# Kernel tuning notes

Measured on AMD Instinct MI355X. Metric: run time of the kernel, lower is better.

The kernel has to match this reference:

```python
import jax, jax.numpy as jnp
import numpy as np

B, D, H, W, L = 32, 768, 14, 14, 77
TEMP_G, TEMP1, TEMP2, TEMP3 = 10.0, 4.0, 5.0, 10.0
LAMBDA_G, LAMBDA_L = 1.0, 1.0
EPS = 1e-8
NEG = -1e30


def setup_inputs() -> dict:
    key = jax.random.key(0)
    k1, k2, k3, k4, k5 = jax.random.split(key, 5)
    img_global = jax.random.normal(k1, (B, D), dtype=jnp.float32)
    img_local = jax.random.normal(k2, (B, D, H, W), dtype=jnp.float32)
    text_global = jax.random.normal(k3, (B, D), dtype=jnp.float32)
    text_local = jax.random.normal(k4, (B, L, D), dtype=jnp.float32)
    # ragged caption lengths: prefix attention mask, lengths in [10, L]
    lens = jax.random.randint(k5, (B,), 10, L + 1)
    attention_mask = (jnp.arange(L)[None, :] < lens[:, None]).astype(jnp.int32)
    return {"img_global": img_global, "img_local": img_local,
            "text_global": text_global, "text_local": text_local,
            "attention_mask": attention_mask}


def _ce_arange(scores):
    # cross entropy with labels = arange(n), mean reduction
    return jnp.mean(jax.nn.logsumexp(scores, axis=1) - jnp.diagonal(scores))


def _gloria_loss(img_global, img_local, text_global, text_local, attention_mask):
    mask = attention_mask.astype(bool)                      # [B, L]
    # ---- global contrastive loss ----
    in_ = img_global / jnp.maximum(jnp.linalg.norm(img_global, axis=1, keepdims=True), 1e-12)
    tn_ = text_global / jnp.maximum(jnp.linalg.norm(text_global, axis=1, keepdims=True), 1e-12)
    g_scores = (in_ @ tn_.T) * TEMP_G                       # [B, B]
    loss_global = 0.5 * (_ce_arange(g_scores) + _ce_arange(g_scores.T))

    # ---- local contrastive loss (vectorized over all text/image pairs) ----
    tl = jnp.swapaxes(text_local, 1, 2)                     # [B, D, L] (forward() transposes since L != D)
    ctx = img_local.reshape(B, D, H * W)                    # [B, D, S]
    # raw attention logits: text i words vs image j pixels -> [i, j, s, l]
    logits = jnp.einsum('jds,idl->ijsl', ctx, tl)
    logits = jnp.where(mask[:, None, None, :], logits, NEG)
    a1 = jax.nn.softmax(logits, axis=-1)                    # softmax over words (first softmax)
    a2 = jax.nn.softmax(TEMP1 * jnp.swapaxes(a1, 2, 3), axis=-1)  # [i, j, l, s], softmax over pixels
    wctx = jnp.einsum('jds,ijls->ijdl', ctx, a2)            # weighted context [i, j, D, l]
    # cosine similarity per word, over feature dim
    w12 = jnp.einsum('idl,ijdl->ijl', tl, wctx)
    n1 = jnp.linalg.norm(tl, axis=1)                        # [i, l]
    n2 = jnp.linalg.norm(wctx, axis=2)                      # [i, j, l]
    cos = w12 / jnp.maximum(n1[:, None, :] * n2, EPS)       # [i, j, l]
    row = jnp.exp(TEMP2 * cos) * mask[:, None, :]           # mask padded words
    sim = jnp.log(row.sum(axis=-1))                         # [i, j]  (local_agg='sum')
    # torch cats per-caption columns: similarities[j, i] -> transpose
    scores = sim.T * TEMP3                                  # [img j, text i]
    loss_local = 0.5 * (_ce_arange(scores) + _ce_arange(scores.T))

    return LAMBDA_G * loss_global + LAMBDA_L * loss_local


def reference(img_global, img_local, text_global, text_local, attention_mask):
    return _gloria_loss(img_global, img_local, text_global, text_local, attention_mask)
```

## Files before the change

kernel.cpp:

```cpp
#include <hip/hip_runtime.h>
#include <math.h>

#define NB 32
#define ND 768
#define NS 196
#define NL 77

typedef __bf16 bf16x8 __attribute__((ext_vector_type(8)));
typedef float f32x4 __attribute__((ext_vector_type(4)));

__device__ __forceinline__ f32x4 mfma16(bf16x8 a, bf16x8 b, f32x4 c) {
  return __builtin_amdgcn_mfma_f32_16x16x32_bf16(a, b, c, 0, 0, 0);
}

#define GLOAD16(gp, lp)                                          \
  __builtin_amdgcn_global_load_lds(                              \
      (const __attribute__((address_space(1))) void*)(gp),       \
      (__attribute__((address_space(3))) void*)(lp), 16, 0, 0)


__global__ __launch_bounds__(256) void prep_all_kernel(
    const float* __restrict__ text_local,
    const float* __restrict__ img_local,
    const int* __restrict__ amask,
    __bf16* __restrict__ txf, __bf16* __restrict__ cTf,
    float* __restrict__ n1ws, int* __restrict__ lenws) {
  const int bid = blockIdx.x;
  const int t = threadIdx.x;
  __shared__ float tile[32][213];

  if (bid < 960) {
    int tau = bid * 256 + t;
    int i = tau / 7680;
    int r = tau - i * 7680;
    int dk = r / 320;
    int r2 = r - dk * 320;
    int lt = r2 >> 6, lane = r2 & 63;
    int n16 = lane & 15, g = lane >> 4;
    int l = lt * 16 + n16;
    float v[8];
#pragma unroll
    for (int q = 0; q < 8; ++q) v[q] = 0.f;
    if (l < NL) {
      const float* src = text_local + ((size_t)i * NL + l) * ND + dk * 32 + g * 8;
      float4 a = *(const float4*)src;
      float4 b = *(const float4*)(src + 4);
      v[0] = a.x; v[1] = a.y; v[2] = a.z; v[3] = a.w;
      v[4] = b.x; v[5] = b.y; v[6] = b.z; v[7] = b.w;
    }
    bf16x8 hv, lv;
#pragma unroll
    for (int q = 0; q < 8; ++q) {
      __bf16 h = (__bf16)v[q];
      hv[q] = h;
      lv[q] = (__bf16)(v[q] - (float)h);
    }
    size_t base = ((((size_t)i * 24 + dk) * 5 + lt) * 2) * 512 + (size_t)lane * 8;
    *(bf16x8*)(txf + base) = hv;
    *(bf16x8*)(txf + base + 512) = lv;
  } else if (bid < 1344) {
    const int b2 = bid - 960;
    const int j = b2 / 12, dc = b2 - (b2 / 12) * 12;
    const float* src = img_local + ((size_t)j * ND + dc * 64) * NS;
#pragma unroll 1
    for (int h = 0; h < 2; ++h) {
      __syncthreads();
      for (int idx = t; idx < 1568; idx += 256) {
        int dd = idx / 49, sq = idx - dd * 49;
        float4 v = *(const float4*)(src + (size_t)(h * 32 + dd) * NS + sq * 4);
        tile[dd][sq * 4 + 0] = v.x;
        tile[dd][sq * 4 + 1] = v.y;
        tile[dd][sq * 4 + 2] = v.z;
        tile[dd][sq * 4 + 3] = v.w;
      }
      __syncthreads();
      const int dk = dc * 2 + h;
      for (int idx = t; idx < 832; idx += 256) {
        int lane = idx & 63;
        int S = idx >> 6;
        int n16 = lane & 15, g = lane >> 4;
        int s = S * 16 + n16;
        bf16x8 hv, lv;
#pragma unroll
        for (int e = 0; e < 8; ++e) {
          float v = (s < NS) ? tile[g * 8 + e][s] : 0.f;
          __bf16 hh = (__bf16)v;
          hv[e] = hh;
          lv[e] = (__bf16)(v - (float)hh);
        }
        size_t base = ((((size_t)j * 13 + S) * 24 + dk) * 2) * 512 + (size_t)lane * 8;
        *(bf16x8*)(cTf + base) = hv;
        *(bf16x8*)(cTf + base + 512) = lv;
      }
    }
  } else {
    const int i = bid - 1344;
    const int lane = t & 63, w = t >> 6;
    __shared__ int slen;
    if (t == 0) slen = 0;
    __syncthreads();
    if (t < NL && amask[i * NL + t] != 0) atomicAdd(&slen, 1);
    for (int l = w; l < NL; l += 4) {
      const float4* p = (const float4*)(text_local + ((size_t)i * NL + l) * ND);
      float s = 0.f;
#pragma unroll
      for (int k = 0; k < 3; ++k) {
        float4 v = p[lane + 64 * k];
        s += v.x * v.x + v.y * v.y + v.z * v.z + v.w * v.w;
      }
#pragma unroll
      for (int off = 32; off; off >>= 1) s += __shfl_xor(s, off);
      if (lane == 0) n1ws[i * 80 + l] = sqrtf(s);
    }
    __syncthreads();
    if (t == 0) lenws[i] = slen;
  }
}

__global__ void mid_kernel(const __bf16* __restrict__ cTf, __bf16* __restrict__ Gf,
                           const float* __restrict__ img_global,
                           const float* __restrict__ text_global,
                           float* __restrict__ gscw,
                           const int* __restrict__ lenws, int* __restrict__ ordws) {
  const int bid = blockIdx.x;
  const int t = threadIdx.x;
  __shared__ __align__(16) float shi[ND];

  if (bid < 832) {
    const int j = bid / 26;
    const int rr = bid - j * 26;
    const int st = rr >> 1, ch = rr & 1;
    const int lane = t & 63, w = t >> 6;
    const int g = lane >> 4, n16 = lane & 15;
    const f32x4 z4 = {0.f, 0.f, 0.f, 0.f};
    f32x4 accG[2];
    accG[0] = z4; accG[1] = z4;
    const int base = ch * 7;
    const int ncols = ch ? 6 : 7;
    const size_t cj = (size_t)j * 13;
    for (int dk = 0; dk < 24; ++dk) {
      size_t ao = ((cj + st) * 24 + dk) * 2 * 512 + (size_t)lane * 8;
      bf16x8 Ah = *(const bf16x8*)(cTf + ao);
      bf16x8 Al = *(const bf16x8*)(cTf + ao + 512);
#pragma unroll
      for (int q = 0; q < 2; ++q) {
        int ntl = w + (q << 2);
        if (ntl < ncols) {
          int nt = base + ntl;
          size_t bo = ((cj + nt) * 24 + dk) * 2 * 512 + (size_t)lane * 8;
          bf16x8 Bh = *(const bf16x8*)(cTf + bo);
          bf16x8 Bl = *(const bf16x8*)(cTf + bo + 512);
          accG[q] = mfma16(Ah, Bh, accG[q]);
          accG[q] = mfma16(Ah, Bl, accG[q]);
          accG[q] = mfma16(Al, Bh, accG[q]);
        }
      }
    }
#pragma unroll
    for (int q = 0; q < 2; ++q) {
      int ntl = w + (q << 2);
      int nt = base + ntl;
      bool compute = (ntl < ncols);
      bool zfill = (ch == 1 && nt == 13);
      if (compute || zfill) {
#pragma unroll
        for (int r = 0; r < 4; ++r) {
          int col = nt * 16 + n16;
          float v = compute ? accG[q][r] : 0.f;
          __bf16 hi = (__bf16)v;
          __bf16 lo = (__bf16)(v - (float)hi);
          int kt = col >> 5, gg = (col >> 3) & 3, e = col & 7;
          int lane2 = (g * 4 + r) + (gg << 4);
          size_t o = ((((size_t)j * 13 + st) * 7 + kt) * 2) * 512 + (size_t)lane2 * 8 + e;
          Gf[o] = hi;
          Gf[o + 512] = lo;
        }
      }
    }
  } else if (bid < 864) {
    const int a = bid - 832;
    const int lane = t & 63, w = t >> 6;
    if (t < ND / 4) ((float4*)shi)[t] = ((const float4*)(img_global + (size_t)a * ND))[t];
    __syncthreads();
    for (int b = w; b < NB; b += 4) {
      const float4* pt = (const float4*)(text_global + (size_t)b * ND);
      const float4* pi = (const float4*)shi;
      float dot = 0.f, ni = 0.f, nt = 0.f;
#pragma unroll
      for (int k = 0; k < 3; ++k) {
        float4 x = pi[lane + 64 * k];
        float4 y = pt[lane + 64 * k];
        dot += x.x * y.x + x.y * y.y + x.z * y.z + x.w * y.w;
        ni  += x.x * x.x + x.y * x.y + x.z * x.z + x.w * x.w;
        nt  += y.x * y.x + y.y * y.y + y.z * y.z + y.w * y.w;
      }
#pragma unroll
      for (int off = 32; off; off >>= 1) {
        dot += __shfl_xor(dot, off);
        ni  += __shfl_xor(ni, off);
        nt  += __shfl_xor(nt, off);
      }
      if (lane == 0)
        gscw[a * NB + b] = dot / fmaxf(sqrtf(ni), 1e-12f) / fmaxf(sqrtf(nt), 1e-12f) * 10.0f;
    }
  } else {
    if (t == 0) {
      int o[32];
      for (int k = 0; k < 32; ++k) o[k] = k;
      for (int x = 0; x < 31; ++x) {
        int best = x;
        for (int y = x + 1; y < 32; ++y)
          if (lenws[o[y]] > lenws[o[best]]) best = y;
        int tmp = o[x]; o[x] = o[best]; o[best] = tmp;
      }
      for (int k = 0; k < 32; ++k) ordws[k] = o[k];
    }
  }
}

__global__ __launch_bounds__(512, 3) void pair_kernel(
    const __bf16* __restrict__ txf, const __bf16* __restrict__ cTf,
    const __bf16* __restrict__ Gf,
    const float* __restrict__ n1ws, const int* __restrict__ lenws,
    const int* __restrict__ ordws,
    float* __restrict__ simws) {
  const int t = threadIdx.x;
  const int wg = ((blockIdx.x & 7) << 6) + (blockIdx.x >> 3);
  const int j = wg >> 4;
  const int m = wg & 15;
  const int i0 = ordws[m], i1 = ordws[31 - m];
  const int len0 = lenws[i0], len1 = lenws[i1];
  const int nlt0 = (len0 + 15) >> 4, nlt1 = (len1 + 15) >> 4;
  const int lane = t & 63, wid = t >> 6;
  const int g = lane >> 4, n16 = lane & 15;
  const bool vb = (wid < 5);

  __shared__ __align__(16) union {
    __bf16 e2f[7 * 5 * 64 * 8];
    __bf16 b1[2][2][5][2][512];
  } U;
  __shared__ float w12s[80], z2s[80], n2s[80];

  const f32x4 z4 = {0.f, 0.f, 0.f, 0.f};
  f32x4 acc[2][2][5];
#pragma unroll
  for (int p = 0; p < 2; ++p)
#pragma unroll
    for (int q = 0; q < 2; ++q)
#pragma unroll
      for (int lt = 0; lt < 5; ++lt) acc[p][q][lt] = z4;

  const __bf16* txi0 = txf + (size_t)i0 * 24 * 5 * 2 * 512;
  const __bf16* txi1 = txf + (size_t)i1 * 24 * 5 * 2 * 512;
  const size_t cj = (size_t)j * 13;

#pragma unroll
  for (int k = 0; k < 4; ++k) {
    int s = wid + ((k & 1) << 3);
    int c = (s < 10) ? s : (s - 10);
    int lt = c >> 1, pl = c & 1;
    const __bf16* tx = (k >> 1) ? txi1 : txi0;
    GLOAD16(tx + (((size_t)lt * 2 + pl) << 9) + ((size_t)lane << 3),
            &U.b1[0][k >> 1][lt][pl][0]);
  }
  __syncthreads();

#pragma unroll 1
  for (int dk = 0; dk < 24; ++dk) {
    const int cur = dk & 1;
    bf16x8 Aha, Ala, Ahb, Alb;
    {
      size_t ao = ((cj + wid) * 24 + dk) * 1024 + ((size_t)lane << 3);
      Aha = *(const bf16x8*)(cTf + ao);
      Ala = *(const bf16x8*)(cTf + ao + 512);
    }
    if (vb) {
      size_t ao = ((cj + wid + 8) * 24 + dk) * 1024 + ((size_t)lane << 3);
      Ahb = *(const bf16x8*)(cTf + ao);
      Alb = *(const bf16x8*)(cTf + ao + 512);
    }
    if (dk < 23) {
#pragma unroll
      for (int k = 0; k < 4; ++k) {
        int s = wid + ((k & 1) << 3);
        int c = (s < 10) ? s : (s - 10);
        int lt = c >> 1, pl = c & 1;
        const __bf16* tx = (k >> 1) ? txi1 : txi0;
        GLOAD16(tx + (((size_t)(dk + 1) * 5 + lt) * 2 + pl) * 512 + ((size_t)lane << 3),
                &U.b1[cur ^ 1][k >> 1][lt][pl][0]);
      }
    }
    __builtin_amdgcn_s_setprio(1);
#pragma unroll
    for (int lt = 0; lt < 5; ++lt) {
      if (lt < nlt0) {
        bf16x8 Bh = *(const bf16x8*)&U.b1[cur][0][lt][0][lane << 3];
        bf16x8 Bl = *(const bf16x8*)&U.b1[cur][0][lt][1][lane << 3];
        acc[0][0][lt] = mfma16(Aha, Bh, acc[0][0][lt]);
        acc[0][0][lt] = mfma16(Aha, Bl, acc[0][0][lt]);
        acc[0][0][lt] = mfma16(Ala, Bh, acc[0][0][lt]);
        if (vb) {
          acc[0][1][lt] = mfma16(Ahb, Bh, acc[0][1][lt]);
          acc[0][1][lt] = mfma16(Ahb, Bl, acc[0][1][lt]);
          acc[0][1][lt] = mfma16(Alb, Bh, acc[0][1][lt]);
        }
      }
      if (lt < nlt1) {
        bf16x8 Bh = *(const bf16x8*)&U.b1[cur][1][lt][0][lane << 3];
        bf16x8 Bl = *(const bf16x8*)&U.b1[cur][1][lt][1][lane << 3];
        acc[1][0][lt] = mfma16(Aha, Bh, acc[1][0][lt]);
        acc[1][0][lt] = mfma16(Aha, Bl, acc[1][0][lt]);
        acc[1][0][lt] = mfma16(Ala, Bh, acc[1][0][lt]);
        if (vb) {
          acc[1][1][lt] = mfma16(Ahb, Bh, acc[1][1][lt]);
          acc[1][1][lt] = mfma16(Ahb, Bl, acc[1][1][lt]);
          acc[1][1][lt] = mfma16(Alb, Bh, acc[1][1][lt]);
        }
      }
    }
    __builtin_amdgcn_s_setprio(0);
    __syncthreads();
  }

#pragma unroll
  for (int p = 0; p < 2; ++p) {
    const int ip   = p ? i1 : i0;
    const int lenp = p ? len1 : len0;
    const int nltp = p ? nlt1 : nlt0;

    __syncthreads();
    if (t < 80) { w12s[t] = 0.f; z2s[t] = 0.f; n2s[t] = 0.f; }
    for (int idx = t; idx < 2240; idx += 512)
      ((uint4*)U.e2f)[idx] = make_uint4(0, 0, 0, 0);
    __syncthreads();

    float w12loc[5], z2loc[5];
#pragma unroll
    for (int lt = 0; lt < 5; ++lt) { w12loc[lt] = 0.f; z2loc[lt] = 0.f; }
#pragma unroll
    for (int q = 0; q < 2; ++q) {
      const int S = wid + (q << 3);
      if (q == 0 || vb) {
#pragma unroll
        for (int r = 0; r < 4; ++r) {
          int s = S * 16 + g * 4 + r;
          bool srow = (s < NS);
          float mx = -1e30f;
#pragma unroll
          for (int lt = 0; lt < 5; ++lt) {
            if (lt < nltp) {
              if ((lt * 16 + n16) < lenp) mx = fmaxf(mx, acc[p][q][lt][r]);
            }
          }
          mx = fmaxf(mx, __shfl_xor(mx, 1));
          mx = fmaxf(mx, __shfl_xor(mx, 2));
          mx = fmaxf(mx, __shfl_xor(mx, 4));
          mx = fmaxf(mx, __shfl_xor(mx, 8));
          float z = 0.f;
          float ev[5];
#pragma unroll
          for (int lt = 0; lt < 5; ++lt) {
            float e = 0.f;
            if (lt < nltp) {
              if ((lt * 16 + n16) < lenp) e = __expf(acc[p][q][lt][r] - mx);
            }
            ev[lt] = e;
            z += e;
          }
          z += __shfl_xor(z, 1);
          z += __shfl_xor(z, 2);
          z += __shfl_xor(z, 4);
          z += __shfl_xor(z, 8);
          float inv = 4.0f / z;
#pragma unroll
          for (int lt = 0; lt < 5; ++lt) {
            if (lt < nltp) {
              if (((lt * 16 + n16) < lenp) && srow) {
                float e2 = __expf(ev[lt] * inv);
                w12loc[lt] += e2 * acc[p][q][lt][r];
                z2loc[lt] += e2;
                int kt = s >> 5, kk = s & 31;
                U.e2f[(((kt * 5) + lt) * 64 + (n16 + ((kk >> 3) << 4))) * 8 + (kk & 7)] = (__bf16)e2;
              }
            }
          }
        }
      }
    }
#pragma unroll
    for (int lt = 0; lt < 5; ++lt) {
      w12loc[lt] += __shfl_xor(w12loc[lt], 16);
      w12loc[lt] += __shfl_xor(w12loc[lt], 32);
      z2loc[lt] += __shfl_xor(z2loc[lt], 16);
      z2loc[lt] += __shfl_xor(z2loc[lt], 32);
    }
    if (lane < 16) {
#pragma unroll
      for (int lt = 0; lt < 5; ++lt) {
        if (lt < nltp) {
          atomicAdd(&w12s[lt * 16 + lane], w12loc[lt]);
          atomicAdd(&z2s[lt * 16 + lane], z2loc[lt]);
        }
      }
    }
    __syncthreads();

    float n2loc[5];
#pragma unroll
    for (int lt = 0; lt < 5; ++lt) n2loc[lt] = 0.f;
#pragma unroll
    for (int q = 0; q < 2; ++q) {
      const int S = wid + (q << 3);
      if (q == 0 || vb) {
        f32x4 a2[5];
#pragma unroll
        for (int lt = 0; lt < 5; ++lt) a2[lt] = z4;
        const __bf16* gp = Gf + (((size_t)j * 13 + S) * 7) * 1024 + ((size_t)lane << 3);
        bf16x8 GAh = *(const bf16x8*)gp;
        bf16x8 GAl = *(const bf16x8*)(gp + 512);
#pragma unroll
        for (int kt = 0; kt < 7; ++kt) {
          bf16x8 GAhN, GAlN;
          if (kt < 6) {
            GAhN = *(const bf16x8*)(gp + (size_t)(kt + 1) * 1024);
            GAlN = *(const bf16x8*)(gp + (size_t)(kt + 1) * 1024 + 512);
          }
          __builtin_amdgcn_s_setprio(1);
#pragma unroll
          for (int lt = 0; lt < 5; ++lt) {
            if (lt < nltp) {
              bf16x8 Bv = *(const bf16x8*)&U.e2f[(((kt * 5) + lt) * 64 + lane) * 8];
              a2[lt] = mfma16(GAh, Bv, a2[lt]);
              a2[lt] = mfma16(GAl, Bv, a2[lt]);
            }
          }
          __builtin_amdgcn_s_setprio(0);
          if (kt < 6) { GAh = GAhN; GAl = GAlN; }
        }
#pragma unroll
        for (int lt = 0; lt < 5; ++lt) {
          if (lt < nltp) {
#pragma unroll
            for (int r = 0; r < 4; ++r) {
              int s = S * 16 + g * 4 + r;
              int kt = s >> 5, kk = s & 31;
              float e2v = (float)U.e2f[(((kt * 5) + lt) * 64 + (n16 + ((kk >> 3) << 4))) * 8 + (kk & 7)];
              n2loc[lt] += e2v * a2[lt][r];
            }
          }
        }
      }
    }
#pragma unroll
    for (int lt = 0; lt < 5; ++lt) {
      n2loc[lt] += __shfl_xor(n2loc[lt], 16);
      n2loc[lt] += __shfl_xor(n2loc[lt], 32);
    }
    if (lane < 16) {
#pragma unroll
      for (int lt = 0; lt < 5; ++lt) {
        if (lt < nltp) atomicAdd(&n2s[lt * 16 + lane], n2loc[lt]);
      }
    }
    __syncthreads();

    if (t < lenp) {
      float z2 = z2s[t];
      float w12v = w12s[t] / z2;
      float n2v = sqrtf(n2s[t]) / z2;
      float n1v = n1ws[ip * 80 + t];
      float cosv = w12v / fmaxf(n1v * n2v, 1e-8f);
      w12s[t] = __expf(5.0f * cosv);
    }
    __syncthreads();
    if (wid == 0) {
      float e = (lane < lenp) ? w12s[lane] : 0.f;
      if (lane + 64 < lenp) e += w12s[lane + 64];
      e += __shfl_xor(e, 1);
      e += __shfl_xor(e, 2);
      e += __shfl_xor(e, 4);
      e += __shfl_xor(e, 8);
      e += __shfl_xor(e, 16);
      e += __shfl_xor(e, 32);
      if (lane == 0) simws[ip * NB + j] = __logf(e);
    }
  }
}

__global__ void loss_kernel(const float* __restrict__ gscw,
                            const float* __restrict__ simws,
                            float* __restrict__ out) {
  const int t = threadIdx.x;
  __shared__ float gs[NB][NB];
  __shared__ float sl[NB][NB];
  __shared__ float parts[4][NB];
  {
    float4 gv = ((const float4*)gscw)[t];
    ((float4*)gs)[t] = gv;
    float4 v = ((const float4*)simws)[t];
    int ii = t >> 3;
    int j0 = (t & 7) * 4;
    sl[j0 + 0][ii] = v.x * 10.0f;
    sl[j0 + 1][ii] = v.y * 10.0f;
    sl[j0 + 2][ii] = v.z * 10.0f;
    sl[j0 + 3][ii] = v.w * 10.0f;
  }
  __syncthreads();
  if (t < NB) {
    float m, z;
    m = -1e30f;
    for (int c = 0; c < NB; ++c) m = fmaxf(m, gs[t][c]);
    z = 0.f;
    for (int c = 0; c < NB; ++c) z += __expf(gs[t][c] - m);
    parts[0][t] = m + __logf(z) - gs[t][t];

    m = -1e30f;
    for (int c = 0; c < NB; ++c) m = fmaxf(m, gs[c][t]);
    z = 0.f;
    for (int c = 0; c < NB; ++c) z += __expf(gs[c][t] - m);
    parts[1][t] = m + __logf(z) - gs[t][t];

    m = -1e30f;
    for (int c = 0; c < NB; ++c) m = fmaxf(m, sl[t][c]);
    z = 0.f;
    for (int c = 0; c < NB; ++c) z += __expf(sl[t][c] - m);
    parts[2][t] = m + __logf(z) - sl[t][t];

    m = -1e30f;
    for (int c = 0; c < NB; ++c) m = fmaxf(m, sl[c][t]);
    z = 0.f;
    for (int c = 0; c < NB; ++c) z += __expf(sl[c][t] - m);
    parts[3][t] = m + __logf(z) - sl[t][t];
  }
  __syncthreads();
  if (t == 0) {
    float s0 = 0.f, s1 = 0.f, s2 = 0.f, s3 = 0.f;
    for (int r = 0; r < NB; ++r) {
      s0 += parts[0][r]; s1 += parts[1][r];
      s2 += parts[2][r]; s3 += parts[3][r];
    }
    out[0] = 0.5f * (s0 + s1) / 32.0f + 0.5f * (s2 + s3) / 32.0f;
  }
}

extern "C" void kernel_launch(void* const* d_in, const int* in_sizes, int n_in,
                              void* d_out, int out_size, void* d_ws, size_t ws_size,
                              hipStream_t stream) {
  (void)in_sizes; (void)n_in; (void)out_size; (void)ws_size;
  const float* img_global  = (const float*)d_in[0];
  const float* img_local   = (const float*)d_in[1];
  const float* text_global = (const float*)d_in[2];
  const float* text_local  = (const float*)d_in[3];
  const int*   amask       = (const int*)d_in[4];

  __bf16* txf = (__bf16*)d_ws;
  __bf16* cTf = txf + (size_t)3932160;
  __bf16* Gf  = cTf + (size_t)10223616;
  float* fsm  = (float*)(Gf + (size_t)2981888);
  float* n1ws  = fsm;
  float* simws = fsm + 2560;
  float* gscw  = fsm + 3584;
  int*   lenws = (int*)(fsm + 4608);
  int*   ordws = (int*)(fsm + 4640);

  prep_all_kernel<<<1376, 256, 0, stream>>>(text_local, img_local, amask,
                                            txf, cTf, n1ws, lenws);
  mid_kernel<<<865, 256, 0, stream>>>(cTf, Gf, img_global, text_global,
                                      gscw, lenws, ordws);
  pair_kernel<<<512, 512, 0, stream>>>(txf, cTf, Gf, n1ws, lenws, ordws, simws);
  loss_kernel<<<1, 256, 0, stream>>>(gscw, simws, (float*)d_out);
}
```

Before: 138.9 us.

## Prefetch A fragments, relax loop barrier, vectorize Gram matrix bf16 stores

The main local kernel now loads the next K-step's A fragments into registers one iteration ahead. It also replaces the full __syncthreads with a vmcnt-limited wait plus a raw barrier, so the prefetched global loads can stay in flight across the barrier. The mid kernel stages its Gram accumulator tile in shared memory and emits the hi/lo bf16 split as 16-byte vector stores instead of scattered 2-byte stores, rebalancing column tiles to 8/5 across the two halves. The hand-coded waitcnt relies on the exact instruction issue order and could expose races if the compiler reorders loads.

```diff
diff --git a/kernel.cpp b/kernel.cpp
--- a/kernel.cpp
+++ b/kernel.cpp
@@ -17,6 +17,8 @@
   __builtin_amdgcn_global_load_lds(                              \
       (const __attribute__((address_space(1))) void*)(gp),       \
       (__attribute__((address_space(3))) void*)(lp), 16, 0, 0)
+
+#define WAITCNT_VM2 (2 | (7 << 4) | (0xF << 8))
 
 
 __global__ __launch_bounds__(256) void prep_all_kernel(
@@ -124,7 +126,7 @@
                            const int* __restrict__ lenws, int* __restrict__ ordws) {
   const int bid = blockIdx.x;
   const int t = threadIdx.x;
-  __shared__ __align__(16) float shi[ND];
+  __shared__ __align__(16) float smem[16 * 132];
 
   if (bid < 832) {
     const int j = bid / 26;
@@ -135,19 +137,17 @@
     const f32x4 z4 = {0.f, 0.f, 0.f, 0.f};
     f32x4 accG[2];
     accG[0] = z4; accG[1] = z4;
-    const int base = ch * 7;
-    const int ncols = ch ? 6 : 7;
+    const int ntbase = ch * 8;
     const size_t cj = (size_t)j * 13;
     for (int dk = 0; dk < 24; ++dk) {
-      size_t ao = ((cj + st) * 24 + dk) * 2 * 512 + (size_t)lane * 8;
+      size_t ao = ((cj + st) * 24 + dk) * 1024 + (size_t)lane * 8;
       bf16x8 Ah = *(const bf16x8*)(cTf + ao);
       bf16x8 Al = *(const bf16x8*)(cTf + ao + 512);
 #pragma unroll
       for (int q = 0; q < 2; ++q) {
-        int ntl = w + (q << 2);
-        if (ntl < ncols) {
-          int nt = base + ntl;
-          size_t bo = ((cj + nt) * 24 + dk) * 2 * 512 + (size_t)lane * 8;
+        int nt = ntbase + w + (q << 2);
+        if (nt <= 12) {
+          size_t bo = ((cj + nt) * 24 + dk) * 1024 + (size_t)lane * 8;
           bf16x8 Bh = *(const bf16x8*)(cTf + bo);
           bf16x8 Bl = *(const bf16x8*)(cTf + bo + 512);
           accG[q] = mfma16(Ah, Bh, accG[q]);
@@ -159,32 +159,37 @@
 #pragma unroll
     for (int q = 0; q < 2; ++q) {
       int ntl = w + (q << 2);
-      int nt = base + ntl;
-      bool compute = (ntl < ncols);
-      bool zfill = (ch == 1 && nt == 13);
-      if (compute || zfill) {
-#pragma unroll
-        for (int r = 0; r < 4; ++r) {
-          int col = nt * 16 + n16;
-          float v = compute ? accG[q][r] : 0.f;
-          __bf16 hi = (__bf16)v;
-          __bf16 lo = (__bf16)(v - (float)hi);
-          int kt = col >> 5, gg = (col >> 3) & 3, e = col & 7;
-          int lane2 = (g * 4 + r) + (gg << 4);
-          size_t o = ((((size_t)j * 13 + st) * 7 + kt) * 2) * 512 + (size_t)lane2 * 8 + e;
-          Gf[o] = hi;
-          Gf[o + 512] = lo;
-        }
-      }
+      int nt = ntbase + ntl;
+      if (nt <= 13) {
+        bool cm = (nt <= 12);
+#pragma unroll
+        for (int r = 0; r < 4; ++r)
+          smem[(g * 4 + r) * 132 + ntl * 16 + n16] = cm ? accG[q][r] : 0.f;
+      }
+    }
+    __syncthreads();
+    const int nkt = ch ? 3 : 4;
+    for (int idx = t; idx < nkt * 128; idx += 256) {
+      int ktl = idx >> 7, pl = (idx >> 6) & 1, ln = idx & 63;
+      int nn = ln & 15, gg = ln >> 4;
+      bf16x8 outv;
+#pragma unroll
+      for (int e = 0; e < 8; ++e) {
+        float v = smem[nn * 132 + ktl * 32 + gg * 8 + e];
+        __bf16 hi = (__bf16)v;
+        outv[e] = pl ? (__bf16)(v - (float)hi) : hi;
+      }
+      int kt = (ch ? 4 : 0) + ktl;
+      *(bf16x8*)(Gf + ((((size_t)j * 13 + st) * 7 + kt) * 2 + pl) * 512 + (size_t)ln * 8) = outv;
     }
   } else if (bid < 864) {
     const int a = bid - 832;
     const int lane = t & 63, w = t >> 6;
-    if (t < ND / 4) ((float4*)shi)[t] = ((const float4*)(img_global + (size_t)a * ND))[t];
+    if (t < ND / 4) ((float4*)smem)[t] = ((const float4*)(img_global + (size_t)a * ND))[t];
     __syncthreads();
     for (int b = w; b < NB; b += 4) {
       const float4* pt = (const float4*)(text_global + (size_t)b * ND);
-      const float4* pi = (const float4*)shi;
+      const float4* pi = (const float4*)smem;
       float dot = 0.f, ni = 0.f, nt = 0.f;
 #pragma unroll
       for (int k = 0; k < 3; ++k) {
@@ -254,6 +259,13 @@
   const __bf16* txi1 = txf + (size_t)i1 * 24 * 5 * 2 * 512;
   const size_t cj = (size_t)j * 13;
 
+  bf16x8 AhaP, AlaP;
+  {
+    size_t ao = ((cj + wid) * 24) * 1024 + ((size_t)lane << 3);
+    AhaP = *(const bf16x8*)(cTf + ao);
+    AlaP = *(const bf16x8*)(cTf + ao + 512);
+  }
+
 #pragma unroll
   for (int k = 0; k < 4; ++k) {
     int s = wid + ((k & 1) << 3);
@@ -268,12 +280,8 @@
 #pragma unroll 1
   for (int dk = 0; dk < 24; ++dk) {
     const int cur = dk & 1;
-    bf16x8 Aha, Ala, Ahb, Alb;
-    {
-      size_t ao = ((cj + wid) * 24 + dk) * 1024 + ((size_t)lane << 3);
-      Aha = *(const bf16x8*)(cTf + ao);
-      Ala = *(const bf16x8*)(cTf + ao + 512);
-    }
+    bf16x8 Aha = AhaP, Ala = AlaP;
+    bf16x8 Ahb, Alb;
     if (vb) {
       size_t ao = ((cj + wid + 8) * 24 + dk) * 1024 + ((size_t)lane << 3);
       Ahb = *(const bf16x8*)(cTf + ao);
@@ -289,6 +297,9 @@
         GLOAD16(tx + (((size_t)(dk + 1) * 5 + lt) * 2 + pl) * 512 + ((size_t)lane << 3),
                 &U.b1[cur ^ 1][k >> 1][lt][pl][0]);
       }
+      size_t ao = ((cj + wid) * 24 + dk + 1) * 1024 + ((size_t)lane << 3);
+      AhaP = *(const bf16x8*)(cTf + ao);
+      AlaP = *(const bf16x8*)(cTf + ao + 512);
     }
     __builtin_amdgcn_s_setprio(1);
 #pragma unroll
@@ -319,7 +330,9 @@
       }
     }
     __builtin_amdgcn_s_setprio(0);
-    __syncthreads();
+    __builtin_amdgcn_s_waitcnt(WAITCNT_VM2);
+    __builtin_amdgcn_s_barrier();
+    __builtin_amdgcn_sched_barrier(0);
   }
 
 #pragma unroll
```

New measurement: 187.1 us. 1.35x slower.
